# Performance work log

Hardware: AMD Instinct MI355X
Metric: run time of the kernel (lower is better)

The kernel has to match this reference:

```python
import jax, jax.numpy as jnp
import numpy as np

E = 8192       # number of edges
D = 256        # edge feature dim


def setup_inputs() -> dict:
    key = jax.random.key(0)
    ks = jax.random.split(key, 4)
    s = 1.0 / np.sqrt(D)
    return {
        "edge_x": jax.random.normal(ks[0], (E, D), dtype=jnp.float32),
        "W_sim1": jax.random.normal(ks[1], (D, D), dtype=jnp.float32) * s,
        "b_sim1": jnp.zeros((D,), dtype=jnp.float32),
        "W_sim2": jax.random.normal(ks[2], (D, D), dtype=jnp.float32) * s,
        "b_sim2": jnp.zeros((D,), dtype=jnp.float32),
        "W_out": jax.random.normal(ks[3], (3 * D, D), dtype=jnp.float32) * (1.0 / np.sqrt(3 * D)),
        "b_out": jnp.zeros((D,), dtype=jnp.float32),
    }


def reference(edge_x, W_sim1, b_sim1, W_sim2, b_sim2, W_out, b_out):
    # MPModule.forward, 'fully' branch.
    # LinearBlock = Linear + ReLU (assumed).
    e1 = jax.nn.relu(edge_x @ W_sim1 + b_sim1)            # [E, D]
    # (e1.unsqueeze(1) * e1).mean(-1)  ==  (e1 @ e1.T) / D, avoiding [E,E,D]
    sim1 = (e1 @ e1.T) / D                                 # [E, E]
    e2 = jax.nn.relu(edge_x @ W_sim2 + b_sim2)             # [E, D]
    sim2 = (e2 @ e2.T) / D                                 # [E, E]
    # (edge_x * sim.unsqueeze(-1)).sum(1) == sim @ edge_x
    agg1 = sim1 @ edge_x                                   # [E, D]
    agg2 = sim2 @ edge_x                                   # [E, D]
    h = jnp.concatenate([edge_x, agg1, agg2], axis=-1)     # [E, 3D]
    return jax.nn.relu(h @ W_out + b_out)                  # [E, D]
```

## Files before the change

### kernel.cpp

```cpp
#include <hip/hip_runtime.h>
#include <hip/hip_bf16.h>


typedef short bf16x8  __attribute__((ext_vector_type(8)));
typedef short short4v __attribute__((ext_vector_type(4)));
typedef float f32x4   __attribute__((ext_vector_type(4)));

__device__ inline short f2bf(float x) {
    unsigned u = __builtin_bit_cast(unsigned, x);
    return (short)((u + 0x7fffu + ((u >> 16) & 1u)) >> 16);
}
__device__ inline float bf2f(short b) {
    return __builtin_bit_cast(float, (unsigned)((unsigned short)b) << 16);
}
__device__ inline void cp16_async(const char* g, char* l) {
    __builtin_amdgcn_global_load_lds(
        (const __attribute__((address_space(1))) unsigned int*)g,
        (__attribute__((address_space(3))) unsigned int*)l, 16, 0, 0);
}

__global__ void prep_all(const float* __restrict__ X, short* __restrict__ h,
                         const float* __restrict__ W1, const float* __restrict__ W2,
                         const float* __restrict__ Wo,
                         short* __restrict__ Wt1, short* __restrict__ Wt2,
                         short* __restrict__ Wto1, short* __restrict__ Wto2,
                         short* __restrict__ Bt4, float* __restrict__ Nacc)
{
    __shared__ short tile[32][33];
    const int tx = threadIdx.x, ty = threadIdx.y;
    if (blockIdx.y < 8) {
        const int r0 = blockIdx.x * 32, c0 = blockIdx.y * 32;
        #pragma unroll
        for (int i = 0; i < 4; ++i) {
            int row = ty + i * 8;
            short b = f2bf(X[(size_t)(r0 + row) * 256 + c0 + tx]);
            int slot = ((((c0 & 32) + tx) >> 3) ^ ((r0 + row) & 7));
            h[(size_t)(r0 + row) * 768 + (c0 & ~63) + slot * 8 + (tx & 7)] = b;
        }
        return;
    }
    int tw = (blockIdx.y - 8) * 256 + blockIdx.x;
    if (tw >= 320) {
        int i0 = (tw - 320) * 256 + ty * 32 + tx;
        for (int i = i0; i < 131072; i += 49152) Nacc[i] = 0.f;
        return;
    }
    const float* src; short* dst; int ldwt, dk0, kx, ny;
    if (tw < 64)       { src = W1; dst = Wt1; ldwt = 256;
                         kx = tw >> 3; ny = tw & 7; dk0 = kx * 32; }
    else if (tw < 128) { int u = tw - 64; src = W2; dst = Wt2; ldwt = 256;
                         kx = u >> 3; ny = u & 7; dk0 = kx * 32; }
    else               { int u = tw - 128; int g = u >> 6; int rem = u & 63;
                         kx = rem >> 3; ny = rem & 7;
                         src = Wo + (size_t)g * 65536;
                         if (g == 0) { dst = Bt4; ldwt = 768; dk0 = kx * 32; }
                         else        { dst = (g == 1) ? Wto1 : Wto2;
                                       ldwt = 256; dk0 = kx * 32; } }
    const int k0l = kx * 32, n0 = ny * 32;
    #pragma unroll
    for (int i = 0; i < 4; ++i) {
        int row = ty + i * 8;
        tile[row][tx] = f2bf(src[(size_t)(k0l + row) * 256 + n0 + tx]);
    }
    __syncthreads();
    #pragma unroll
    for (int i = 0; i < 4; ++i) {
        int row = ty + i * 8;
        int n = n0 + row;
        int slot = ((((dk0 & 32) + tx) >> 3) ^ (n & 7));
        dst[(size_t)n * ldwt + (dk0 & ~63) + slot * 8 + (tx & 7)] = tile[tx][row];
    }
}

__global__ __launch_bounds__(256, 1)
void gemm_all(int job, short* __restrict__ h,
              const short* __restrict__ Wt1, const short* __restrict__ Wt2,
              const short* __restrict__ Wto1, const short* __restrict__ Wto2,
              const short* __restrict__ Bt4,
              const float* __restrict__ b1, const float* __restrict__ b2,
              const float* __restrict__ bo,
              short* __restrict__ e1t, short* __restrict__ e2t,
              short* __restrict__ G1t, short* __restrict__ G2t,
              float* __restrict__ Nacc, float* __restrict__ outf)
{
    const int z = blockIdx.z;
    int mode, sim = 0, kbeg = 0, kend, lda, ldb;
    const short *Ap, *Bp;
    const float* bias = nullptr;
    short* et = nullptr;
    if (job == 0) {
        Ap = h; lda = 768; kend = 256; ldb = 256;
        if (z < 2) { mode = 1; sim = z;     Bp = z ? Wt2 : Wt1;
                     bias = z ? b2 : b1;    et = z ? e2t : e1t; }
        else       { mode = 3; sim = z - 2; Bp = sim ? Wto2 : Wto1;
                     et = sim ? G2t : G1t; }
    } else if (job == 1) {
        mode = 2; sim = z & 1;
        kbeg = (z >> 1) * 512; kend = kbeg + 512;
        Ap = sim ? G2t : G1t; lda = 8192;
        Bp = sim ? e2t : e1t; ldb = 8192;
    } else {
        mode = 0; Ap = h; lda = 768; kend = 768;
        Bp = Bt4; ldb = 768; bias = bo;
    }

    const int m0 = blockIdx.x * 128, n0 = blockIdx.y * 128;
    const int t = threadIdx.x;
    const int w = t >> 6, l = t & 63, lr = l & 15, q = l >> 4;
    const int wm = w >> 1, wn = w & 1;
    const int wub = t & ~63;

    __shared__ __attribute__((aligned(16))) short S[2][2][128 * 64];

    f32x4 acc[4][4];
    #pragma unroll
    for (int i = 0; i < 4; ++i)
        #pragma unroll
        for (int j = 0; j < 4; ++j) acc[i][j] = f32x4{0.f, 0.f, 0.f, 0.f};

    auto stage = [&](int buf, int k0) {
        #pragma unroll
        for (int it = 0; it < 4; ++it) {
            int idx = it * 256 + t;
            int r = idx >> 3, s = idx & 7;
            cp16_async((const char*)(Ap + (size_t)(m0 + r) * lda + k0) + s * 16,
                       (char*)&S[buf][0][0] + (size_t)(it * 256 + wub) * 16);
        }
        #pragma unroll
        for (int it = 0; it < 4; ++it) {
            int idx = it * 256 + t;
            int r = idx >> 3, s = idx & 7;
            cp16_async((const char*)(Bp + (size_t)(n0 + r) * ldb + k0) + s * 16,
                       (char*)&S[buf][1][0] + (size_t)(it * 256 + wub) * 16);
        }
    };

    stage(0, kbeg);
    __syncthreads();
    int cur = 0;
    for (int k0 = kbeg; k0 < kend; k0 += 64) {
        if (k0 + 64 < kend) stage(cur ^ 1, k0 + 64);
        const short* As = &S[cur][0][0];
        const short* Bs = &S[cur][1][0];
        #pragma unroll
        for (int ks = 0; ks < 2; ++ks) {
            bf16x8 af[4], bfr[4];
            #pragma unroll
            for (int mt = 0; mt < 4; ++mt) {
                int ar = wm * 64 + mt * 16 + lr;
                af[mt] = *(const bf16x8*)&As[ar * 64 + (((ks*4 + q) ^ (ar & 7)) << 3)];
            }
            #pragma unroll
            for (int nt = 0; nt < 4; ++nt) {
                int br = wn * 64 + nt * 16 + lr;
                bfr[nt] = *(const bf16x8*)&Bs[br * 64 + (((ks*4 + q) ^ (br & 7)) << 3)];
            }
            #pragma unroll
            for (int mt = 0; mt < 4; ++mt)
                #pragma unroll
                for (int nt = 0; nt < 4; ++nt)
                    acc[mt][nt] = __builtin_amdgcn_mfma_f32_16x16x32_bf16(
                        af[mt], bfr[nt], acc[mt][nt], 0, 0, 0);
        }
        __syncthreads();
        cur ^= 1;
    }

    if (mode == 0) {
        #pragma unroll
        for (int mt = 0; mt < 4; ++mt)
            #pragma unroll
            for (int nt = 0; nt < 4; ++nt)
                #pragma unroll
                for (int r = 0; r < 4; ++r) {
                    int m = m0 + wm * 64 + mt * 16 + q * 4 + r;
                    int n = n0 + wn * 64 + nt * 16 + lr;
                    float v = acc[mt][nt][r] + bias[n];
                    outf[(size_t)m * 256 + n] = v > 0.f ? v : 0.f;
                }
    } else if (mode == 2) {
        float* Mo = Nacc + (size_t)sim * 65536;
        #pragma unroll
        for (int mt = 0; mt < 4; ++mt)
            #pragma unroll
            for (int nt = 0; nt < 4; ++nt)
                #pragma unroll
                for (int r = 0; r < 4; ++r) {
                    int m = m0 + wm * 64 + mt * 16 + q * 4 + r;
                    int n = n0 + wn * 64 + nt * 16 + lr;
                    atomicAdd(&Mo[(size_t)m * 256 + n],
                              acc[mt][nt][r] * (1.0f / 256.0f));
                }
    } else {
        short* Hs = &S[0][0][0];
        short* Ts = &S[1][0][0];
        #pragma unroll
        for (int mt = 0; mt < 4; ++mt)
            #pragma unroll
            for (int nt = 0; nt < 4; ++nt) {
                int n_loc = wn * 64 + nt * 16 + lr;
                float bb = (mode == 1) ? bias[n0 + n_loc] : 0.f;
                short vb[4];
                #pragma unroll
                for (int r = 0; r < 4; ++r) {
                    float v = acc[mt][nt][r] + bb;
                    if (mode == 1) v = v > 0.f ? v : 0.f;
                    vb[r] = f2bf(v);
                    if (mode == 1) {
                        int m_loc = wm * 64 + mt * 16 + q * 4 + r;
                        Hs[m_loc * 128 + n_loc] = vb[r];
                    }
                }
                int gm = wm * 8 + mt * 2 + (q >> 1);
                short4v pk = { vb[0], vb[1], vb[2], vb[3] };
                *(short4v*)&Ts[n_loc * 128 + ((gm >> 3) << 6)
                               + (((gm & 7) ^ (n_loc & 7)) << 3) + ((q & 1) << 2)] = pk;
            }
        __syncthreads();
        if (mode == 1) {
            const int cb = 256 + sim * 256 + n0;
            for (int i = t; i < 2048; i += 256) {
                int ml = i >> 4, g = i & 15;
                bf16x8 hv = *(const bf16x8*)&Hs[ml * 128 + g * 8];
                *(bf16x8*)(h + (size_t)(m0 + ml) * 768 + cb + ((g >> 3) << 6)
                           + (((g & 7) ^ (ml & 7)) << 3)) = hv;
            }
        }
        for (int i = t; i < 2048; i += 256) {
            int nl = i >> 4, s = i & 15;
            bf16x8 tv = *(const bf16x8*)&Ts[nl * 128 + s * 8];
            *(bf16x8*)(et + (size_t)(n0 + nl) * 8192 + m0 + s * 8) = tv;
        }
    }
}

__global__ void convert_n(const float* __restrict__ Nacc, short* __restrict__ Bt4)
{
    int gid = blockIdx.x * 256 + threadIdx.x;
    int sim = gid >> 13, rem = gid & 8191;
    int n = rem >> 5, g = rem & 31;
    const float* np = Nacc + (size_t)sim * 65536 + (size_t)n * 256 + g * 8;
    f32x4 va = *(const f32x4*)np;
    f32x4 vb = *(const f32x4*)(np + 4);
    bf16x8 pk;
    pk[0] = f2bf(va[0]); pk[1] = f2bf(va[1]);
    pk[2] = f2bf(va[2]); pk[3] = f2bf(va[3]);
    pk[4] = f2bf(vb[0]); pk[5] = f2bf(vb[1]);
    pk[6] = f2bf(vb[2]); pk[7] = f2bf(vb[3]);
    int k = 256 + sim * 256 + g * 8;
    int slot = (g & 7) ^ (n & 7);
    *(bf16x8*)(Bt4 + (size_t)n * 768 + (k & ~63) + slot * 8) = pk;
}

extern "C" void kernel_launch(void* const* d_in, const int* in_sizes, int n_in,
                              void* d_out, int out_size, void* d_ws, size_t ws_size,
                              hipStream_t stream)
{
    const float* edge_x = (const float*)d_in[0];
    const float* W1 = (const float*)d_in[1];
    const float* b1 = (const float*)d_in[2];
    const float* W2 = (const float*)d_in[3];
    const float* b2 = (const float*)d_in[4];
    const float* Wo = (const float*)d_in[5];
    const float* bo = (const float*)d_in[6];

    char* ws = (char*)d_ws;
    short* h    = (short*)ws;
    short* e1t  = (short*)(ws + 12582912);
    short* e2t  = (short*)(ws + 16777216);
    short* G1t  = (short*)(ws + 20971520);
    short* G2t  = (short*)(ws + 25165824);
    short* Wt1  = (short*)(ws + 29360128);
    short* Wt2  = (short*)(ws + 29491200);
    short* Wto1 = (short*)(ws + 29622272);
    short* Wto2 = (short*)(ws + 29753344);
    short* Bt4  = (short*)(ws + 29884416);
    float* Nacc = (float*)(ws + 30277632);

    float* out = (float*)d_out;

    prep_all<<<dim3(256, 10), dim3(32, 8), 0, stream>>>(
        edge_x, h, W1, W2, Wo, Wt1, Wt2, Wto1, Wto2, Bt4, Nacc);

    gemm_all<<<dim3(64, 2, 4), 256, 0, stream>>>(
        0, h, Wt1, Wt2, Wto1, Wto2, Bt4, b1, b2, bo,
        e1t, e2t, G1t, G2t, Nacc, out);

    gemm_all<<<dim3(2, 2, 32), 256, 0, stream>>>(
        1, h, Wt1, Wt2, Wto1, Wto2, Bt4, b1, b2, bo,
        e1t, e2t, G1t, G2t, Nacc, out);

    convert_n<<<dim3(64), 256, 0, stream>>>(Nacc, Bt4);

    gemm_all<<<dim3(64, 2, 1), 256, 0, stream>>>(
        2, h, Wt1, Wt2, Wto1, Wto2, Bt4, b1, b2, bo,
        e1t, e2t, G1t, G2t, Nacc, out);
}
```

Before: 114.1 us.

## Fuse all stages into one cooperative persistent kernel with grid syncs

Replaces the five separate launches (prep, first GEMMs, reassociated NxN GEMM, convert, output GEMM) with a single cooperative kernel whose phases are separated by grid-wide syncs. Blocks loop over job indices per phase. The final GEMM now uses smaller 64x64 tiles so more blocks have work. The aim is to remove launch gaps and tail effects between small kernels, at the cost of grid-sync overhead and one fixed persistent grid size. The old multi-launch path stays as a fallback if the cooperative launch fails.

Result: no change. 114.7 us (+0.6%).

```diff
diff --git a/kernel.cpp b/kernel.cpp
--- a/kernel.cpp
+++ b/kernel.cpp
@@ -1,5 +1,8 @@
 #include <hip/hip_runtime.h>
 #include <hip/hip_bf16.h>
+#include <hip/hip_cooperative_groups.h>
+
+namespace cg = cooperative_groups;
 
 
 typedef short bf16x8  __attribute__((ext_vector_type(8)));
@@ -18,6 +21,290 @@
         (const __attribute__((address_space(1))) unsigned int*)g,
         (__attribute__((address_space(3))) unsigned int*)l, 16, 0, 0);
 }
+
+__device__ __forceinline__ void core128(
+    const short* __restrict__ Ap, int lda, const short* __restrict__ Bp, int ldb,
+    int kbeg, int kend, int m0, int n0, short* Sf, f32x4 acc[4][4], int t)
+{
+    const int l = t & 63, lr = l & 15, q = l >> 4;
+    const int w = t >> 6, wm = w >> 1, wn = w & 1;
+    const int wub = t & ~63;
+
+    auto stage = [&](int buf, int k0) {
+        #pragma unroll
+        for (int it = 0; it < 4; ++it) {
+            int idx = it * 256 + t, r = idx >> 3, s = idx & 7;
+            cp16_async((const char*)(Ap + (size_t)(m0 + r) * lda + k0) + s * 16,
+                       (char*)(Sf + buf * 16384) + (size_t)(it * 256 + wub) * 16);
+        }
+        #pragma unroll
+        for (int it = 0; it < 4; ++it) {
+            int idx = it * 256 + t, r = idx >> 3, s = idx & 7;
+            cp16_async((const char*)(Bp + (size_t)(n0 + r) * ldb + k0) + s * 16,
+                       (char*)(Sf + buf * 16384 + 8192) + (size_t)(it * 256 + wub) * 16);
+        }
+    };
+
+    stage(0, kbeg);
+    __syncthreads();
+    int cur = 0;
+    for (int k0 = kbeg; k0 < kend; k0 += 64) {
+        if (k0 + 64 < kend) stage(cur ^ 1, k0 + 64);
+        const short* As = Sf + cur * 16384;
+        const short* Bs = As + 8192;
+        #pragma unroll
+        for (int ks = 0; ks < 2; ++ks) {
+            bf16x8 af[4], bfr[4];
+            #pragma unroll
+            for (int mt = 0; mt < 4; ++mt) {
+                int ar = wm * 64 + mt * 16 + lr;
+                af[mt] = *(const bf16x8*)&As[ar * 64 + (((ks*4 + q) ^ (ar & 7)) << 3)];
+            }
+            #pragma unroll
+            for (int nt = 0; nt < 4; ++nt) {
+                int br = wn * 64 + nt * 16 + lr;
+                bfr[nt] = *(const bf16x8*)&Bs[br * 64 + (((ks*4 + q) ^ (br & 7)) << 3)];
+            }
+            #pragma unroll
+            for (int mt = 0; mt < 4; ++mt)
+                #pragma unroll
+                for (int nt = 0; nt < 4; ++nt)
+                    acc[mt][nt] = __builtin_amdgcn_mfma_f32_16x16x32_bf16(
+                        af[mt], bfr[nt], acc[mt][nt], 0, 0, 0);
+        }
+        __syncthreads();
+        cur ^= 1;
+    }
+}
+
+__global__ __launch_bounds__(256, 1)
+void mpnn_fused(int NB, const float* __restrict__ X,
+                const float* __restrict__ W1, const float* __restrict__ b1v,
+                const float* __restrict__ W2, const float* __restrict__ b2v,
+                const float* __restrict__ Wo, const float* __restrict__ bov,
+                short* __restrict__ h, short* __restrict__ e1t, short* __restrict__ e2t,
+                short* __restrict__ G1t, short* __restrict__ G2t,
+                short* __restrict__ Wt1, short* __restrict__ Wt2,
+                short* __restrict__ Wto1, short* __restrict__ Wto2,
+                short* __restrict__ Bt4, float* __restrict__ Nacc,
+                float* __restrict__ outf)
+{
+    cg::grid_group gg = cg::this_grid();
+    const int b = blockIdx.x, t = threadIdx.x;
+    const int l = t & 63, lr = l & 15, q = l >> 4;
+    const int w = t >> 6, wm = w >> 1, wn = w & 1, wub = t & ~63;
+
+    __shared__ __attribute__((aligned(16))) short S[4][8192];
+    short* Sf = &S[0][0];
+
+    {
+        for (int gi = b * 256 + t; gi < 262144; gi += NB * 256) {
+            int r = gi >> 5, g = gi & 31;
+            const float* xp = X + (size_t)r * 256 + g * 8;
+            f32x4 va = *(const f32x4*)xp;
+            f32x4 vb = *(const f32x4*)(xp + 4);
+            bf16x8 pk;
+            pk[0] = f2bf(va[0]); pk[1] = f2bf(va[1]);
+            pk[2] = f2bf(va[2]); pk[3] = f2bf(va[3]);
+            pk[4] = f2bf(vb[0]); pk[5] = f2bf(vb[1]);
+            pk[6] = f2bf(vb[2]); pk[7] = f2bf(vb[3]);
+            int slot = (g & 7) ^ (r & 7);
+            *(bf16x8*)(h + (size_t)r * 768 + (g >> 3) * 64 + slot * 8) = pk;
+        }
+        for (int i = b * 256 + t; i < 131072; i += NB * 256) Nacc[i] = 0.f;
+        short (*tile)[33] = (short(*)[33])Sf;
+        const int tx = t & 31, ty = t >> 5;
+        for (int tw = b; tw < 320; tw += NB) {
+            const float* src; short* dst; int ldwt, dk0, kx, ny;
+            if (tw < 64)       { src = W1; dst = Wt1; ldwt = 256;
+                                 kx = tw >> 3; ny = tw & 7; dk0 = kx * 32; }
+            else if (tw < 128) { int u = tw - 64; src = W2; dst = Wt2; ldwt = 256;
+                                 kx = u >> 3; ny = u & 7; dk0 = kx * 32; }
+            else               { int u = tw - 128; int g = u >> 6; int rem = u & 63;
+                                 kx = rem >> 3; ny = rem & 7;
+                                 src = Wo + (size_t)g * 65536;
+                                 if (g == 0) { dst = Bt4; ldwt = 768; dk0 = kx * 32; }
+                                 else        { dst = (g == 1) ? Wto1 : Wto2;
+                                               ldwt = 256; dk0 = kx * 32; } }
+            const int k0l = kx * 32, n0 = ny * 32;
+            __syncthreads();
+            #pragma unroll
+            for (int i = 0; i < 4; ++i) {
+                int row = ty + i * 8;
+                tile[row][tx] = f2bf(src[(size_t)(k0l + row) * 256 + n0 + tx]);
+            }
+            __syncthreads();
+            #pragma unroll
+            for (int i = 0; i < 4; ++i) {
+                int row = ty + i * 8;
+                int n = n0 + row;
+                int slot = ((((dk0 & 32) + tx) >> 3) ^ (n & 7));
+                dst[(size_t)n * ldwt + (dk0 & ~63) + slot * 8 + (tx & 7)] =
+                    tile[tx][row];
+            }
+        }
+    }
+    gg.sync();
+
+    for (int job = b; job < 512; job += NB) {
+        const int z = job >> 7, rem = job & 127;
+        const int m0 = (rem & 63) * 128, n0 = (rem >> 6) * 128;
+        const int mode = (z < 2) ? 1 : 3;
+        const int sim = z & 1;
+        const short* Bp   = (z == 0) ? Wt1 : (z == 1) ? Wt2 : (z == 2) ? Wto1 : Wto2;
+        const float* bias = (z == 0) ? b1v : (z == 1) ? b2v : nullptr;
+        short* et         = (z == 0) ? e1t : (z == 1) ? e2t : (z == 2) ? G1t : G2t;
+
+        __syncthreads();
+        f32x4 acc[4][4];
+        #pragma unroll
+        for (int i = 0; i < 4; ++i)
+            #pragma unroll
+            for (int j = 0; j < 4; ++j) acc[i][j] = f32x4{0.f, 0.f, 0.f, 0.f};
+        core128(h, 768, Bp, 256, 0, 256, m0, n0, Sf, acc, t);
+
+        short* Hs = Sf;
+        short* Ts = Sf + 16384;
+        #pragma unroll
+        for (int mt = 0; mt < 4; ++mt)
+            #pragma unroll
+            for (int nt = 0; nt < 4; ++nt) {
+                int n_loc = wn * 64 + nt * 16 + lr;
+                float bb = (mode == 1) ? bias[n0 + n_loc] : 0.f;
+                short vb[4];
+                #pragma unroll
+                for (int r = 0; r < 4; ++r) {
+                    float v = acc[mt][nt][r] + bb;
+                    if (mode == 1) v = v > 0.f ? v : 0.f;
+                    vb[r] = f2bf(v);
+                    if (mode == 1) {
+                        int m_loc = wm * 64 + mt * 16 + q * 4 + r;
+                        Hs[m_loc * 128 + n_loc] = vb[r];
+                    }
+                }
+                int gm = wm * 8 + mt * 2 + (q >> 1);
+                short4v pk = { vb[0], vb[1], vb[2], vb[3] };
+                *(short4v*)&Ts[n_loc * 128 + ((gm >> 3) << 6)
+                               + (((gm & 7) ^ (n_loc & 7)) << 3) + ((q & 1) << 2)] = pk;
+            }
+        __syncthreads();
+        if (mode == 1) {
+            const int cb = 256 + sim * 256 + n0;
+            for (int i = t; i < 2048; i += 256) {
+                int ml = i >> 4, g = i & 15;
+                bf16x8 hv = *(const bf16x8*)&Hs[ml * 128 + g * 8];
+                *(bf16x8*)(h + (size_t)(m0 + ml) * 768 + cb + ((g >> 3) << 6)
+                           + (((g & 7) ^ (ml & 7)) << 3)) = hv;
+            }
+        }
+        for (int i = t; i < 2048; i += 256) {
+            int nl = i >> 4, s = i & 15;
+            bf16x8 tv = *(const bf16x8*)&Ts[nl * 128 + s * 8];
+            *(bf16x8*)(et + (size_t)(n0 + nl) * 8192 + m0 + s * 8) = tv;
+        }
+    }
+    gg.sync();
+
+    for (int job = b; job < 128; job += NB) {
+        const int bx = job & 1, by = (job >> 1) & 1, bz = job >> 2;
+        const int sim = bz & 1, split = bz >> 1;
+        const int kbeg = split * 512, kend = kbeg + 512;
+        const int m0 = bx * 128, n0 = by * 128;
+        const short* Ap = sim ? G2t : G1t;
+        const short* Bp = sim ? e2t : e1t;
+
+        __syncthreads();
+        f32x4 acc[4][4];
+        #pragma unroll
+        for (int i = 0; i < 4; ++i)
+            #pragma unroll
+            for (int j = 0; j < 4; ++j) acc[i][j] = f32x4{0.f, 0.f, 0.f, 0.f};
+        core128(Ap, 8192, Bp, 8192, kbeg, kend, m0, n0, Sf, acc, t);
+
+        float* Mo = Nacc + (size_t)sim * 65536;
+        #pragma unroll
+        for (int mt = 0; mt < 4; ++mt)
+            #pragma unroll
+            for (int nt = 0; nt < 4; ++nt)
+                #pragma unroll
+                for (int r = 0; r < 4; ++r) {
+                    int m = m0 + wm * 64 + mt * 16 + q * 4 + r;
+                    int n = n0 + wn * 64 + nt * 16 + lr;
+                    atomicAdd(&Mo[(size_t)m * 256 + n],
+                              acc[mt][nt][r] * (1.0f / 256.0f));
+                }
+    }
+    gg.sync();
+
+    for (int job = b; job < 64; job += NB) {
+        int gid = job * 256 + t;
+        int sim = gid >> 13, rem = gid & 8191;
+        int n = rem >> 5, g = rem & 31;
+        const float* np = Nacc + (size_t)sim * 65536 + (size_t)n * 256 + g * 8;
+        f32x4 va = *(const f32x4*)np;
+        f32x4 vb = *(const f32x4*)(np + 4);
+        bf16x8 pk;
+        pk[0] = f2bf(va[0]); pk[1] = f2bf(va[1]);
+        pk[2] = f2bf(va[2]); pk[3] = f2bf(va[3]);
+        pk[4] = f2bf(vb[0]); pk[5] = f2bf(vb[1]);
+        pk[6] = f2bf(vb[2]); pk[7] = f2bf(vb[3]);
+        int k = 256 + sim * 256 + g * 8;
+        int slot = (g & 7) ^ (n & 7);
+        *(bf16x8*)(Bt4 + (size_t)n * 768 + (k & ~63) + slot * 8) = pk;
+    }
+    gg.sync();
+
+    {
+        short* As = Sf;
+        short* Bs = Sf + 4096;
+        for (int job = b; job < 512; job += NB) {
+            const int m0 = (job >> 2) * 64, n0 = (job & 3) * 64;
+            f32x4 acc4[4];
+            #pragma unroll
+            for (int i = 0; i < 4; ++i) acc4[i] = f32x4{0.f, 0.f, 0.f, 0.f};
+            for (int k0 = 0; k0 < 768; k0 += 64) {
+                __syncthreads();
+                #pragma unroll
+                for (int it = 0; it < 2; ++it) {
+                    int idx = it * 256 + t, r = idx >> 3, s = idx & 7;
+                    cp16_async((const char*)(h + (size_t)(m0 + r) * 768 + k0) + s * 16,
+                               (char*)As + (size_t)(it * 256 + wub) * 16);
+                }
+                #pragma unroll
+                for (int it = 0; it < 2; ++it) {
+                    int idx = it * 256 + t, r = idx >> 3, s = idx & 7;
+                    cp16_async((const char*)(Bt4 + (size_t)(n0 + r) * 768 + k0) + s * 16,
+                               (char*)Bs + (size_t)(it * 256 + wub) * 16);
+                }
+                __syncthreads();
+                #pragma unroll
+                for (int ks = 0; ks < 2; ++ks) {
+                    int arow = w * 16 + lr;
+                    bf16x8 af = *(const bf16x8*)
+                        &As[arow * 64 + (((ks*4 + q) ^ (arow & 7)) << 3)];
+                    #pragma unroll
+                    for (int nt = 0; nt < 4; ++nt) {
+                        int brow = nt * 16 + lr;
+                        bf16x8 bfg = *(const bf16x8*)
+                            &Bs[brow * 64 + (((ks*4 + q) ^ (brow & 7)) << 3)];
+                        acc4[nt] = __builtin_amdgcn_mfma_f32_16x16x32_bf16(
+                            af, bfg, acc4[nt], 0, 0, 0);
+                    }
+                }
+            }
+            #pragma unroll
+            for (int nt = 0; nt < 4; ++nt)
+                #pragma unroll
+                for (int r = 0; r < 4; ++r) {
+                    int m = m0 + w * 16 + q * 4 + r;
+                    int n = n0 + nt * 16 + lr;
+                    float v = acc4[nt][r] + bov[n];
+                    outf[(size_t)m * 256 + n] = v > 0.f ? v : 0.f;
+                }
+        }
+    }
+}
+
 
 __global__ void prep_all(const float* __restrict__ X, short* __restrict__ h,
                          const float* __restrict__ W1, const float* __restrict__ W2,
@@ -106,11 +393,11 @@
 
     const int m0 = blockIdx.x * 128, n0 = blockIdx.y * 128;
     const int t = threadIdx.x;
-    const int w = t >> 6, l = t & 63, lr = l & 15, q = l >> 4;
-    const int wm = w >> 1, wn = w & 1;
-    const int wub = t & ~63;
-
-    __shared__ __attribute__((aligned(16))) short S[2][2][128 * 64];
+    const int l = t & 63, lr = l & 15, q = l >> 4;
+    const int w = t >> 6, wm = w >> 1, wn = w & 1;
+
+    __shared__ __attribute__((aligned(16))) short S[4][8192];
+    short* Sf = &S[0][0];
 
     f32x4 acc[4][4];
     #pragma unroll
@@ -118,53 +405,7 @@
         #pragma unroll
         for (int j = 0; j < 4; ++j) acc[i][j] = f32x4{0.f, 0.f, 0.f, 0.f};
 
-    auto stage = [&](int buf, int k0) {
-        #pragma unroll
-        for (int it = 0; it < 4; ++it) {
-            int idx = it * 256 + t;
-            int r = idx >> 3, s = idx & 7;
-            cp16_async((const char*)(Ap + (size_t)(m0 + r) * lda + k0) + s * 16,
-                       (char*)&S[buf][0][0] + (size_t)(it * 256 + wub) * 16);
-        }
-        #pragma unroll
-        for (int it = 0; it < 4; ++it) {
-            int idx = it * 256 + t;
-            int r = idx >> 3, s = idx & 7;
-            cp16_async((const char*)(Bp + (size_t)(n0 + r) * ldb + k0) + s * 16,
-                       (char*)&S[buf][1][0] + (size_t)(it * 256 + wub) * 16);
-        }
-    };
-
-    stage(0, kbeg);
-    __syncthreads();
-    int cur = 0;
-    for (int k0 = kbeg; k0 < kend; k0 += 64) {
-        if (k0 + 64 < kend) stage(cur ^ 1, k0 + 64);
-        const short* As = &S[cur][0][0];
-        const short* Bs = &S[cur][1][0];
-        #pragma unroll
-        for (int ks = 0; ks < 2; ++ks) {
-            bf16x8 af[4], bfr[4];
-            #pragma unroll
-            for (int mt = 0; mt < 4; ++mt) {
-                int ar = wm * 64 + mt * 16 + lr;
-                af[mt] = *(const bf16x8*)&As[ar * 64 + (((ks*4 + q) ^ (ar & 7)) << 3)];
-            }
-            #pragma unroll
-            for (int nt = 0; nt < 4; ++nt) {
-                int br = wn * 64 + nt * 16 + lr;
-                bfr[nt] = *(const bf16x8*)&Bs[br * 64 + (((ks*4 + q) ^ (br & 7)) << 3)];
-            }
-            #pragma unroll
-            for (int mt = 0; mt < 4; ++mt)
-                #pragma unroll
-                for (int nt = 0; nt < 4; ++nt)
-                    acc[mt][nt] = __builtin_amdgcn_mfma_f32_16x16x32_bf16(
-                        af[mt], bfr[nt], acc[mt][nt], 0, 0, 0);
-        }
-        __syncthreads();
-        cur ^= 1;
-    }
+    core128(Ap, lda, Bp, ldb, kbeg, kend, m0, n0, Sf, acc, t);
 
     if (mode == 0) {
         #pragma unroll
@@ -192,8 +433,8 @@
                               acc[mt][nt][r] * (1.0f / 256.0f));
                 }
     } else {
-        short* Hs = &S[0][0][0];
-        short* Ts = &S[1][0][0];
+        short* Hs = Sf;
+        short* Ts = Sf + 16384;
         #pragma unroll
         for (int mt = 0; mt < 4; ++mt)
             #pragma unroll
@@ -279,19 +520,31 @@
 
     float* out = (float*)d_out;
 
+    int nbpm = 0;
+    hipError_t oe = hipOccupancyMaxActiveBlocksPerMultiprocessor(
+        &nbpm, (const void*)mpnn_fused, 256, 0);
+    if (oe == hipSuccess && nbpm >= 1) {
+        int NB = (nbpm >= 2) ? 512 : 256;
+        void* args[] = { &NB, (void*)&edge_x, (void*)&W1, (void*)&b1,
+                         (void*)&W2, (void*)&b2, (void*)&Wo, (void*)&bo,
+                         (void*)&h, (void*)&e1t, (void*)&e2t, (void*)&G1t,
+                         (void*)&G2t, (void*)&Wt1, (void*)&Wt2, (void*)&Wto1,
+                         (void*)&Wto2, (void*)&Bt4, (void*)&Nacc, (void*)&out };
+        hipError_t le = hipLaunchCooperativeKernel(
+            (const void*)mpnn_fused, dim3(NB, 1, 1), dim3(256, 1, 1),
+            args, 0, stream);
+        if (le == hipSuccess) return;
+    }
+
     prep_all<<<dim3(256, 10), dim3(32, 8), 0, stream>>>(
         edge_x, h, W1, W2, Wo, Wt1, Wt2, Wto1, Wto2, Bt4, Nacc);
-
     gemm_all<<<dim3(64, 2, 4), 256, 0, stream>>>(
         0, h, Wt1, Wt2, Wto1, Wto2, Bt4, b1, b2, bo,
         e1t, e2t, G1t, G2t, Nacc, out);
-
     gemm_all<<<dim3(2, 2, 32), 256, 0, stream>>>(
         1, h, Wt1, Wt2, Wto1, Wto2, Bt4, b1, b2, bo,
         e1t, e2t, G1t, G2t, Nacc, out);
-
     convert_n<<<dim3(64), 256, 0, stream>>>(Nacc, Bt4);
-
     gemm_all<<<dim3(64, 2, 1), 256, 0, stream>>>(
         2, h, Wt1, Wt2, Wto1, Wto2, Bt4, b1, b2, bo,
         e1t, e2t, G1t, G2t, Nacc, out);
```

## Fuse prep into first GEMM and merge reduction, convert, and output GEMM via grid barriers

Applied to the files above, without the earlier changes.

Drops the separate prep kernel. The first GEMM now loads fp32 X and the weights directly, converts them to bf16 on the fly into LDS, and writes the bf16 copy of X into h. The split-K atomics into Nacc are replaced by per-split slabs. A single persistent 128-block kernel computes the partial products, then uses atomic-ticket grid barriers to reduce the slabs, convert them to bf16, and run the output GEMM. This cuts five launches to two and removes the atomics and zero-initialisation, at the cost of spin barriers and register-staged conversion in the inner loop, which could limit overlap. The ticket reset in the first kernel relies on stream ordering between the two kernels.

New measurement: 140.6 us. 23.3% more time.

```diff
diff --git a/kernel.cpp b/kernel.cpp
--- a/kernel.cpp
+++ b/kernel.cpp
@@ -19,119 +19,26 @@
         (__attribute__((address_space(3))) unsigned int*)l, 16, 0, 0);
 }
 
-__global__ void prep_all(const float* __restrict__ X, short* __restrict__ h,
-                         const float* __restrict__ W1, const float* __restrict__ W2,
-                         const float* __restrict__ Wo,
-                         short* __restrict__ Wt1, short* __restrict__ Wt2,
-                         short* __restrict__ Wto1, short* __restrict__ Wto2,
-                         short* __restrict__ Bt4, float* __restrict__ Nacc)
+__device__ __forceinline__ void core128(
+    const short* __restrict__ Ap, int lda, const short* __restrict__ Bp, int ldb,
+    int kbeg, int kend, int m0, int n0, short* Sf, f32x4 acc[4][4], int t)
 {
-    __shared__ short tile[32][33];
-    const int tx = threadIdx.x, ty = threadIdx.y;
-    if (blockIdx.y < 8) {
-        const int r0 = blockIdx.x * 32, c0 = blockIdx.y * 32;
-        #pragma unroll
-        for (int i = 0; i < 4; ++i) {
-            int row = ty + i * 8;
-            short b = f2bf(X[(size_t)(r0 + row) * 256 + c0 + tx]);
-            int slot = ((((c0 & 32) + tx) >> 3) ^ ((r0 + row) & 7));
-            h[(size_t)(r0 + row) * 768 + (c0 & ~63) + slot * 8 + (tx & 7)] = b;
-        }
-        return;
-    }
-    int tw = (blockIdx.y - 8) * 256 + blockIdx.x;
-    if (tw >= 320) {
-        int i0 = (tw - 320) * 256 + ty * 32 + tx;
-        for (int i = i0; i < 131072; i += 49152) Nacc[i] = 0.f;
-        return;
-    }
-    const float* src; short* dst; int ldwt, dk0, kx, ny;
-    if (tw < 64)       { src = W1; dst = Wt1; ldwt = 256;
-                         kx = tw >> 3; ny = tw & 7; dk0 = kx * 32; }
-    else if (tw < 128) { int u = tw - 64; src = W2; dst = Wt2; ldwt = 256;
-                         kx = u >> 3; ny = u & 7; dk0 = kx * 32; }
-    else               { int u = tw - 128; int g = u >> 6; int rem = u & 63;
-                         kx = rem >> 3; ny = rem & 7;
-                         src = Wo + (size_t)g * 65536;
-                         if (g == 0) { dst = Bt4; ldwt = 768; dk0 = kx * 32; }
-                         else        { dst = (g == 1) ? Wto1 : Wto2;
-                                       ldwt = 256; dk0 = kx * 32; } }
-    const int k0l = kx * 32, n0 = ny * 32;
-    #pragma unroll
-    for (int i = 0; i < 4; ++i) {
-        int row = ty + i * 8;
-        tile[row][tx] = f2bf(src[(size_t)(k0l + row) * 256 + n0 + tx]);
-    }
-    __syncthreads();
-    #pragma unroll
-    for (int i = 0; i < 4; ++i) {
-        int row = ty + i * 8;
-        int n = n0 + row;
-        int slot = ((((dk0 & 32) + tx) >> 3) ^ (n & 7));
-        dst[(size_t)n * ldwt + (dk0 & ~63) + slot * 8 + (tx & 7)] = tile[tx][row];
-    }
-}
-
-__global__ __launch_bounds__(256, 1)
-void gemm_all(int job, short* __restrict__ h,
-              const short* __restrict__ Wt1, const short* __restrict__ Wt2,
-              const short* __restrict__ Wto1, const short* __restrict__ Wto2,
-              const short* __restrict__ Bt4,
-              const float* __restrict__ b1, const float* __restrict__ b2,
-              const float* __restrict__ bo,
-              short* __restrict__ e1t, short* __restrict__ e2t,
-              short* __restrict__ G1t, short* __restrict__ G2t,
-              float* __restrict__ Nacc, float* __restrict__ outf)
-{
-    const int z = blockIdx.z;
-    int mode, sim = 0, kbeg = 0, kend, lda, ldb;
-    const short *Ap, *Bp;
-    const float* bias = nullptr;
-    short* et = nullptr;
-    if (job == 0) {
-        Ap = h; lda = 768; kend = 256; ldb = 256;
-        if (z < 2) { mode = 1; sim = z;     Bp = z ? Wt2 : Wt1;
-                     bias = z ? b2 : b1;    et = z ? e2t : e1t; }
-        else       { mode = 3; sim = z - 2; Bp = sim ? Wto2 : Wto1;
-                     et = sim ? G2t : G1t; }
-    } else if (job == 1) {
-        mode = 2; sim = z & 1;
-        kbeg = (z >> 1) * 512; kend = kbeg + 512;
-        Ap = sim ? G2t : G1t; lda = 8192;
-        Bp = sim ? e2t : e1t; ldb = 8192;
-    } else {
-        mode = 0; Ap = h; lda = 768; kend = 768;
-        Bp = Bt4; ldb = 768; bias = bo;
-    }
-
-    const int m0 = blockIdx.x * 128, n0 = blockIdx.y * 128;
-    const int t = threadIdx.x;
-    const int w = t >> 6, l = t & 63, lr = l & 15, q = l >> 4;
-    const int wm = w >> 1, wn = w & 1;
+    const int l = t & 63, lr = l & 15, q = l >> 4;
+    const int w = t >> 6, wm = w >> 1, wn = w & 1;
     const int wub = t & ~63;
 
-    __shared__ __attribute__((aligned(16))) short S[2][2][128 * 64];
-
-    f32x4 acc[4][4];
-    #pragma unroll
-    for (int i = 0; i < 4; ++i)
-        #pragma unroll
-        for (int j = 0; j < 4; ++j) acc[i][j] = f32x4{0.f, 0.f, 0.f, 0.f};
-
     auto stage = [&](int buf, int k0) {
         #pragma unroll
         for (int it = 0; it < 4; ++it) {
-            int idx = it * 256 + t;
-            int r = idx >> 3, s = idx & 7;
+            int idx = it * 256 + t, r = idx >> 3, s = idx & 7;
             cp16_async((const char*)(Ap + (size_t)(m0 + r) * lda + k0) + s * 16,
-                       (char*)&S[buf][0][0] + (size_t)(it * 256 + wub) * 16);
+                       (char*)(Sf + buf * 16384) + (size_t)(it * 256 + wub) * 16);
         }
         #pragma unroll
         for (int it = 0; it < 4; ++it) {
-            int idx = it * 256 + t;
-            int r = idx >> 3, s = idx & 7;
+            int idx = it * 256 + t, r = idx >> 3, s = idx & 7;
             cp16_async((const char*)(Bp + (size_t)(n0 + r) * ldb + k0) + s * 16,
-                       (char*)&S[buf][1][0] + (size_t)(it * 256 + wub) * 16);
+                       (char*)(Sf + buf * 16384 + 8192) + (size_t)(it * 256 + wub) * 16);
         }
     };
 
@@ -140,8 +47,8 @@
     int cur = 0;
     for (int k0 = kbeg; k0 < kend; k0 += 64) {
         if (k0 + 64 < kend) stage(cur ^ 1, k0 + 64);
-        const short* As = &S[cur][0][0];
-        const short* Bs = &S[cur][1][0];
+        const short* As = Sf + cur * 16384;
+        const short* Bs = As + 8192;
         #pragma unroll
         for (int ks = 0; ks < 2; ++ks) {
             bf16x8 af[4], bfr[4];
@@ -165,8 +72,206 @@
         __syncthreads();
         cur ^= 1;
     }
-
-    if (mode == 0) {
+}
+
+__global__ __launch_bounds__(256, 1)
+void d1_eg(const float* __restrict__ X,
+           const float* __restrict__ W1, const float* __restrict__ b1v,
+           const float* __restrict__ W2, const float* __restrict__ b2v,
+           const float* __restrict__ Wo,
+           short* __restrict__ h, short* __restrict__ e1t, short* __restrict__ e2t,
+           short* __restrict__ G1t, short* __restrict__ G2t,
+           short* __restrict__ Bt4, int* __restrict__ ticket)
+{
+    const int bx = blockIdx.x, by = blockIdx.y, z = blockIdx.z;
+    const int t = threadIdx.x;
+    const int l = t & 63, lr = l & 15, q = l >> 4;
+    const int w = t >> 6, wm = w >> 1, wn = w & 1;
+
+    if (bx == 0 && by == 0 && z == 0 && t == 0) { ticket[0] = 0; ticket[1] = 0; }
+
+    __shared__ __attribute__((aligned(16))) short S[32768];
+
+    if (z == 2 && by == 0) {
+        short (*tile)[33] = (short(*)[33])S;
+        const int tx = t & 31, ty = t >> 5;
+        const int kx = bx >> 3, ny = bx & 7;
+        const int dk0 = kx * 32, k0l = kx * 32, n0l = ny * 32;
+        #pragma unroll
+        for (int i = 0; i < 4; ++i) {
+            int row = ty + i * 8;
+            tile[row][tx] = f2bf(Wo[(size_t)(k0l + row) * 256 + n0l + tx]);
+        }
+        __syncthreads();
+        #pragma unroll
+        for (int i = 0; i < 4; ++i) {
+            int row = ty + i * 8;
+            int n = n0l + row;
+            int slot = ((((dk0 & 32) + tx) >> 3) ^ (n & 7));
+            Bt4[(size_t)n * 768 + (dk0 & ~63) + slot * 8 + (tx & 7)] = tile[tx][row];
+        }
+        __syncthreads();
+    }
+
+    const float* Wz   = (z == 0) ? W1 : (z == 1) ? W2 : (Wo + (size_t)(z - 1) * 65536);
+    const float* bias = (z == 0) ? b1v : (z == 1) ? b2v : nullptr;
+    short* et         = (z == 0) ? e1t : (z == 1) ? e2t : (z == 2) ? G1t : G2t;
+    const int  mode   = (z < 2) ? 1 : 3;
+    const int  sim    = z & 1;
+    const bool writeX = (z == 0 && by == 0);
+    const int m0 = bx * 128, n0 = by * 128;
+
+    f32x4 acc[4][4];
+    #pragma unroll
+    for (int i = 0; i < 4; ++i)
+        #pragma unroll
+        for (int j = 0; j < 4; ++j) acc[i][j] = f32x4{0.f, 0.f, 0.f, 0.f};
+
+    f32x4 ra[4][2];
+    float rb[4][8];
+
+    auto loadAB = [&](int k0) {
+        #pragma unroll
+        for (int i = 0; i < 4; ++i) {
+            int idx = i * 256 + t, r = idx >> 3, g = idx & 7;
+            const float* xp = X + (size_t)(m0 + r) * 256 + k0 + g * 8;
+            ra[i][0] = *(const f32x4*)xp;
+            ra[i][1] = *(const f32x4*)(xp + 4);
+        }
+        #pragma unroll
+        for (int i = 0; i < 4; ++i) {
+            int idx = i * 256 + t, n = idx & 127, g = idx >> 7;
+            const float* wp = Wz + (size_t)(k0 + g * 8) * 256 + n0 + n;
+            #pragma unroll
+            for (int j = 0; j < 8; ++j) rb[i][j] = wp[(size_t)j * 256];
+        }
+    };
+    auto writeAB = [&](int buf, int k0) {
+        #pragma unroll
+        for (int i = 0; i < 4; ++i) {
+            int idx = i * 256 + t, r = idx >> 3, g = idx & 7;
+            bf16x8 pk;
+            pk[0] = f2bf(ra[i][0][0]); pk[1] = f2bf(ra[i][0][1]);
+            pk[2] = f2bf(ra[i][0][2]); pk[3] = f2bf(ra[i][0][3]);
+            pk[4] = f2bf(ra[i][1][0]); pk[5] = f2bf(ra[i][1][1]);
+            pk[6] = f2bf(ra[i][1][2]); pk[7] = f2bf(ra[i][1][3]);
+            *(bf16x8*)&S[buf * 16384 + r * 64 + ((g ^ (r & 7)) << 3)] = pk;
+            if (writeX)
+                *(bf16x8*)(h + (size_t)(m0 + r) * 768 + k0 + ((g ^ (r & 7)) << 3)) = pk;
+        }
+        #pragma unroll
+        for (int i = 0; i < 4; ++i) {
+            int idx = i * 256 + t, n = idx & 127, g = idx >> 7;
+            bf16x8 pk;
+            #pragma unroll
+            for (int j = 0; j < 8; ++j) pk[j] = f2bf(rb[i][j]);
+            *(bf16x8*)&S[buf * 16384 + 8192 + n * 64 + ((g ^ (n & 7)) << 3)] = pk;
+        }
+    };
+
+    loadAB(0);
+    writeAB(0, 0);
+    __syncthreads();
+    int cur = 0;
+    for (int k0 = 0; k0 < 256; k0 += 64) {
+        const bool nx = (k0 + 64 < 256);
+        if (nx) loadAB(k0 + 64);
+        const short* As = S + cur * 16384;
+        const short* Bs = As + 8192;
+        #pragma unroll
+        for (int ks = 0; ks < 2; ++ks) {
+            bf16x8 af[4], bfr[4];
+            #pragma unroll
+            for (int mt = 0; mt < 4; ++mt) {
+                int ar = wm * 64 + mt * 16 + lr;
+                af[mt] = *(const bf16x8*)&As[ar * 64 + (((ks*4 + q) ^ (ar & 7)) << 3)];
+            }
+            #pragma unroll
+            for (int nt = 0; nt < 4; ++nt) {
+                int br = wn * 64 + nt * 16 + lr;
+                bfr[nt] = *(const bf16x8*)&Bs[br * 64 + (((ks*4 + q) ^ (br & 7)) << 3)];
+            }
+            #pragma unroll
+            for (int mt = 0; mt < 4; ++mt)
+                #pragma unroll
+                for (int nt = 0; nt < 4; ++nt)
+                    acc[mt][nt] = __builtin_amdgcn_mfma_f32_16x16x32_bf16(
+                        af[mt], bfr[nt], acc[mt][nt], 0, 0, 0);
+        }
+        if (nx) writeAB(cur ^ 1, k0 + 64);
+        __syncthreads();
+        cur ^= 1;
+    }
+
+    short* Hs = S;
+    short* Ts = S + 16384;
+    #pragma unroll
+    for (int mt = 0; mt < 4; ++mt)
+        #pragma unroll
+        for (int nt = 0; nt < 4; ++nt) {
+            int n_loc = wn * 64 + nt * 16 + lr;
+            float bb = (mode == 1) ? bias[n0 + n_loc] : 0.f;
+            short vb[4];
+            #pragma unroll
+            for (int r = 0; r < 4; ++r) {
+                float v = acc[mt][nt][r] + bb;
+                if (mode == 1) v = v > 0.f ? v : 0.f;
+                vb[r] = f2bf(v);
+                if (mode == 1) {
+                    int m_loc = wm * 64 + mt * 16 + q * 4 + r;
+                    Hs[m_loc * 128 + n_loc] = vb[r];
+                }
+            }
+            int gm = wm * 8 + mt * 2 + (q >> 1);
+            short4v pk = { vb[0], vb[1], vb[2], vb[3] };
+            *(short4v*)&Ts[n_loc * 128 + ((gm >> 3) << 6)
+                           + (((gm & 7) ^ (n_loc & 7)) << 3) + ((q & 1) << 2)] = pk;
+        }
+    __syncthreads();
+    if (mode == 1) {
+        const int cb = 256 + sim * 256 + n0;
+        for (int i = t; i < 2048; i += 256) {
+            int ml = i >> 4, g = i & 15;
+            bf16x8 hv = *(const bf16x8*)&Hs[ml * 128 + g * 8];
+            *(bf16x8*)(h + (size_t)(m0 + ml) * 768 + cb + ((g >> 3) << 6)
+                       + (((g & 7) ^ (ml & 7)) << 3)) = hv;
+        }
+    }
+    for (int i = t; i < 2048; i += 256) {
+        int nl = i >> 4, s = i & 15;
+        bf16x8 tv = *(const bf16x8*)&Ts[nl * 128 + s * 8];
+        *(bf16x8*)(et + (size_t)(n0 + nl) * 8192 + m0 + s * 8) = tv;
+    }
+}
+
+__global__ __launch_bounds__(256, 1)
+void d23(const short* __restrict__ e1t, const short* __restrict__ e2t,
+         const short* __restrict__ G1t, const short* __restrict__ G2t,
+         const short* __restrict__ h, short* __restrict__ Bt4,
+         float* __restrict__ Nslab, int* __restrict__ ticket,
+         const float* __restrict__ bov, float* __restrict__ outf)
+{
+    const int fb = blockIdx.x, t = threadIdx.x;
+    const int l = t & 63, lr = l & 15, q = l >> 4;
+    const int w = t >> 6, wm = w >> 1, wn = w & 1;
+
+    __shared__ __attribute__((aligned(16))) short S[32768];
+
+    {
+        const int bx = fb & 1, by = (fb >> 1) & 1, bz = fb >> 2;
+        const int sim = bz & 1, split = bz >> 1;
+        const int kbeg = split * 512, m0 = bx * 128, n0 = by * 128;
+        const short* Ap = sim ? G2t : G1t;
+        const short* Bp = sim ? e2t : e1t;
+
+        f32x4 acc[4][4];
+        #pragma unroll
+        for (int i = 0; i < 4; ++i)
+            #pragma unroll
+            for (int j = 0; j < 4; ++j) acc[i][j] = f32x4{0.f, 0.f, 0.f, 0.f};
+        core128(Ap, 8192, Bp, 8192, kbeg, kbeg + 512, m0, n0, S, acc, t);
+
+        float* Mo = Nslab + (size_t)(split * 2 + sim) * 65536;
         #pragma unroll
         for (int mt = 0; mt < 4; ++mt)
             #pragma unroll
@@ -175,11 +280,61 @@
                 for (int r = 0; r < 4; ++r) {
                     int m = m0 + wm * 64 + mt * 16 + q * 4 + r;
                     int n = n0 + wn * 64 + nt * 16 + lr;
-                    float v = acc[mt][nt][r] + bias[n];
-                    outf[(size_t)m * 256 + n] = v > 0.f ? v : 0.f;
+                    Mo[(size_t)m * 256 + n] = acc[mt][nt][r] * (1.0f / 256.0f);
                 }
-    } else if (mode == 2) {
-        float* Mo = Nacc + (size_t)sim * 65536;
+    }
+
+    __syncthreads();
+    if (t == 0) {
+        __threadfence();
+        __hip_atomic_fetch_add(&ticket[0], 1, __ATOMIC_ACQ_REL, __HIP_MEMORY_SCOPE_AGENT);
+        while (__hip_atomic_load(&ticket[0], __ATOMIC_ACQUIRE, __HIP_MEMORY_SCOPE_AGENT) < 128)
+            __builtin_amdgcn_s_sleep(8);
+    }
+    __syncthreads();
+    __threadfence();
+
+    if (t < 128) {
+        int gid = fb * 128 + t;
+        int simg = gid >> 13, rem = gid & 8191;
+        int n = rem >> 5, g = rem & 31;
+        f32x4 sa = f32x4{0.f, 0.f, 0.f, 0.f}, sb = f32x4{0.f, 0.f, 0.f, 0.f};
+        #pragma unroll
+        for (int s = 0; s < 16; ++s) {
+            const float* np = Nslab + (size_t)(s * 2 + simg) * 65536
+                              + (size_t)n * 256 + g * 8;
+            sa += *(const f32x4*)np;
+            sb += *(const f32x4*)(np + 4);
+        }
+        bf16x8 pk;
+        pk[0] = f2bf(sa[0]); pk[1] = f2bf(sa[1]);
+        pk[2] = f2bf(sa[2]); pk[3] = f2bf(sa[3]);
+        pk[4] = f2bf(sb[0]); pk[5] = f2bf(sb[1]);
+        pk[6] = f2bf(sb[2]); pk[7] = f2bf(sb[3]);
+        int k = 256 + simg * 256 + g * 8;
+        int slot = (g & 7) ^ (n & 7);
+        *(bf16x8*)(Bt4 + (size_t)n * 768 + (k & ~63) + slot * 8) = pk;
+    }
+
+    __syncthreads();
+    if (t == 0) {
+        __threadfence();
+        __hip_atomic_fetch_add(&ticket[1], 1, __ATOMIC_ACQ_REL, __HIP_MEMORY_SCOPE_AGENT);
+        while (__hip_atomic_load(&ticket[1], __ATOMIC_ACQUIRE, __HIP_MEMORY_SCOPE_AGENT) < 128)
+            __builtin_amdgcn_s_sleep(8);
+    }
+    __syncthreads();
+    __threadfence();
+
+    {
+        const int m0 = (fb >> 1) * 128, n0 = (fb & 1) * 128;
+        f32x4 acc[4][4];
+        #pragma unroll
+        for (int i = 0; i < 4; ++i)
+            #pragma unroll
+            for (int j = 0; j < 4; ++j) acc[i][j] = f32x4{0.f, 0.f, 0.f, 0.f};
+        core128(h, 768, Bt4, 768, 0, 768, m0, n0, S, acc, t);
+
         #pragma unroll
         for (int mt = 0; mt < 4; ++mt)
             #pragma unroll
@@ -188,68 +343,10 @@
                 for (int r = 0; r < 4; ++r) {
                     int m = m0 + wm * 64 + mt * 16 + q * 4 + r;
                     int n = n0 + wn * 64 + nt * 16 + lr;
-                    atomicAdd(&Mo[(size_t)m * 256 + n],
-                              acc[mt][nt][r] * (1.0f / 256.0f));
+                    float v = acc[mt][nt][r] + bov[n];
+                    outf[(size_t)m * 256 + n] = v > 0.f ? v : 0.f;
                 }
-    } else {
-        short* Hs = &S[0][0][0];
-        short* Ts = &S[1][0][0];
-        #pragma unroll
-        for (int mt = 0; mt < 4; ++mt)
-            #pragma unroll
-            for (int nt = 0; nt < 4; ++nt) {
-                int n_loc = wn * 64 + nt * 16 + lr;
-                float bb = (mode == 1) ? bias[n0 + n_loc] : 0.f;
-                short vb[4];
-                #pragma unroll
-                for (int r = 0; r < 4; ++r) {
-                    float v = acc[mt][nt][r] + bb;
-                    if (mode == 1) v = v > 0.f ? v : 0.f;
-                    vb[r] = f2bf(v);
-                    if (mode == 1) {
-                        int m_loc = wm * 64 + mt * 16 + q * 4 + r;
-                        Hs[m_loc * 128 + n_loc] = vb[r];
-                    }
-                }
-                int gm = wm * 8 + mt * 2 + (q >> 1);
-                short4v pk = { vb[0], vb[1], vb[2], vb[3] };
-                *(short4v*)&Ts[n_loc * 128 + ((gm >> 3) << 6)
-                               + (((gm & 7) ^ (n_loc & 7)) << 3) + ((q & 1) << 2)] = pk;
-            }
-        __syncthreads();
-        if (mode == 1) {
-            const int cb = 256 + sim * 256 + n0;
-            for (int i = t; i < 2048; i += 256) {
-                int ml = i >> 4, g = i & 15;
-                bf16x8 hv = *(const bf16x8*)&Hs[ml * 128 + g * 8];
-                *(bf16x8*)(h + (size_t)(m0 + ml) * 768 + cb + ((g >> 3) << 6)
-                           + (((g & 7) ^ (ml & 7)) << 3)) = hv;
-            }
-        }
-        for (int i = t; i < 2048; i += 256) {
-            int nl = i >> 4, s = i & 15;
-            bf16x8 tv = *(const bf16x8*)&Ts[nl * 128 + s * 8];
-            *(bf16x8*)(et + (size_t)(n0 + nl) * 8192 + m0 + s * 8) = tv;
-        }
-    }
-}
-
-__global__ void convert_n(const float* __restrict__ Nacc, short* __restrict__ Bt4)
-{
-    int gid = blockIdx.x * 256 + threadIdx.x;
-    int sim = gid >> 13, rem = gid & 8191;
-    int n = rem >> 5, g = rem & 31;
-    const float* np = Nacc + (size_t)sim * 65536 + (size_t)n * 256 + g * 8;
-    f32x4 va = *(const f32x4*)np;
-    f32x4 vb = *(const f32x4*)(np + 4);
-    bf16x8 pk;
-    pk[0] = f2bf(va[0]); pk[1] = f2bf(va[1]);
-    pk[2] = f2bf(va[2]); pk[3] = f2bf(va[3]);
-    pk[4] = f2bf(vb[0]); pk[5] = f2bf(vb[1]);
-    pk[6] = f2bf(vb[2]); pk[7] = f2bf(vb[3]);
-    int k = 256 + sim * 256 + g * 8;
-    int slot = (g & 7) ^ (n & 7);
-    *(bf16x8*)(Bt4 + (size_t)n * 768 + (k & ~63) + slot * 8) = pk;
+    }
 }
 
 extern "C" void kernel_launch(void* const* d_in, const int* in_sizes, int n_in,
@@ -265,34 +362,20 @@
     const float* bo = (const float*)d_in[6];
 
     char* ws = (char*)d_ws;
-    short* h    = (short*)ws;
-    short* e1t  = (short*)(ws + 12582912);
-    short* e2t  = (short*)(ws + 16777216);
-    short* G1t  = (short*)(ws + 20971520);
-    short* G2t  = (short*)(ws + 25165824);
-    short* Wt1  = (short*)(ws + 29360128);
-    short* Wt2  = (short*)(ws + 29491200);
-    short* Wto1 = (short*)(ws + 29622272);
-    short* Wto2 = (short*)(ws + 29753344);
-    short* Bt4  = (short*)(ws + 29884416);
-    float* Nacc = (float*)(ws + 30277632);
+    short* h     = (short*)ws;
+    short* e1t   = (short*)(ws + 12582912);
+    short* e2t   = (short*)(ws + 16777216);
+    short* G1t   = (short*)(ws + 20971520);
+    short* G2t   = (short*)(ws + 25165824);
+    short* Bt4   = (short*)(ws + 29360128);
+    float* Nslab = (float*)(ws + 29753344);
+    int*   tick  = (int*)(ws + 38141952);
 
     float* out = (float*)d_out;
 
-    prep_all<<<dim3(256, 10), dim3(32, 8), 0, stream>>>(
-        edge_x, h, W1, W2, Wo, Wt1, Wt2, Wto1, Wto2, Bt4, Nacc);
-
-    gemm_all<<<dim3(64, 2, 4), 256, 0, stream>>>(
-        0, h, Wt1, Wt2, Wto1, Wto2, Bt4, b1, b2, bo,
-        e1t, e2t, G1t, G2t, Nacc, out);
-
-    gemm_all<<<dim3(2, 2, 32), 256, 0, stream>>>(
-        1, h, Wt1, Wt2, Wto1, Wto2, Bt4, b1, b2, bo,
-        e1t, e2t, G1t, G2t, Nacc, out);
-
-    convert_n<<<dim3(64), 256, 0, stream>>>(Nacc, Bt4);
-
-    gemm_all<<<dim3(64, 2, 1), 256, 0, stream>>>(
-        2, h, Wt1, Wt2, Wto1, Wto2, Bt4, b1, b2, bo,
-        e1t, e2t, G1t, G2t, Nacc, out);
-}
+    d1_eg<<<dim3(64, 2, 4), 256, 0, stream>>>(
+        edge_x, W1, b1, W2, b2, Wo, h, e1t, e2t, G1t, G2t, Bt4, tick);
+
+    d23<<<dim3(128), 256, 0, stream>>>(
+        e1t, e2t, G1t, G2t, h, Bt4, Nslab, tick, bo, out);
+}
```
